# Performance work log

Measured on AMD Instinct MI355X. Metric: run time of the kernel, lower is better.

The kernel has to match this reference:

```python
import jax, jax.numpy as jnp
import numpy as np
from jax import lax

DIM = 192
HEADS = 4
EPS = 1e-12  # torch F.normalize eps


def setup_inputs() -> dict:
    key = jax.random.key(0)
    k1, k2, k3, k4 = jax.random.split(key, 4)
    b, c, h, w = 8, DIM, 128, 128
    x = jax.random.normal(k1, (b, c, h, w), dtype=jnp.float32)
    w_qkv = jax.random.normal(k2, (3 * c, c), dtype=jnp.float32) * (1.0 / np.sqrt(c))
    w_dw = jax.random.normal(k3, (3 * c, 1, 3, 3), dtype=jnp.float32) * (1.0 / 3.0)
    temperature = jnp.ones((HEADS, 1, 1), dtype=jnp.float32)
    w_proj = jax.random.normal(k4, (c, c), dtype=jnp.float32) * (1.0 / np.sqrt(c))
    return {"x": x, "w_qkv": w_qkv, "w_dw": w_dw, "temperature": temperature, "w_proj": w_proj}


def _l2norm(t):
    # torch F.normalize(dim=-1): t / max(||t||_2, eps)
    n = jnp.sqrt(jnp.sum(t * t, axis=-1, keepdims=True))
    return t / jnp.maximum(n, EPS)


def reference(x, w_qkv, w_dw, temperature, w_proj):
    b, c, h, w = x.shape
    heads = HEADS
    hc = c // heads  # channels per head
    # 1x1 conv: dim -> 3*dim
    qkv = jnp.einsum('bchw,oc->bohw', x, w_qkv)
    # depthwise 3x3 conv, padding=1, no relu/norm
    qkv = lax.conv_general_dilated(
        qkv, w_dw, window_strides=(1, 1), padding='SAME',
        feature_group_count=3 * c,
        dimension_numbers=('NCHW', 'OIHW', 'NCHW'))
    q, k, v = jnp.split(qkv, 3, axis=1)
    # b (head c) h w -> b head c (h w)
    n = h * w
    q = q.reshape(b, heads, hc, n)
    k = k.reshape(b, heads, hc, n)
    v = v.reshape(b, heads, hc, n)
    q = _l2norm(q)
    k = _l2norm(k)
    # channel attention: [b, head, hc, hc]
    attn = jnp.einsum('bhcn,bhdn->bhcd', q, k) * temperature[None]
    attn = jax.nn.softmax(attn, axis=-1)
    out = jnp.einsum('bhcd,bhdn->bhcn', attn, v)
    out = out.reshape(b, c, h, w)
    out = jnp.einsum('bchw,oc->bohw', out, w_proj)
    return out
```

## Files before the change

kernel.cpp:

```cpp
#include <hip/hip_runtime.h>
#include <stdint.h>


typedef __attribute__((ext_vector_type(8))) short bf16x8;
typedef __attribute__((ext_vector_type(4))) float f32x4;
typedef __attribute__((ext_vector_type(2))) float f32x2;
typedef __attribute__((ext_vector_type(4))) unsigned int u32x4;
typedef __attribute__((ext_vector_type(2))) unsigned int u32x2;
typedef unsigned short u16;

#define HW 16384
#define CD 192
#define O3 576
#define KD 192

__device__ __forceinline__ float b2f(u16 u) {
    union { unsigned int i; float f; } v; v.i = ((unsigned int)u) << 16; return v.f;
}
__device__ __forceinline__ u16 f2b(float f) {
    union { float f; unsigned int i; } v; v.f = f;
    return (u16)((v.i + 0x7fffu + ((v.i >> 16) & 1u)) >> 16);
}

__global__ __launch_bounds__(256) void fill_f32(float* p, long long n, float val) {
    long long stride = (long long)gridDim.x * 256;
    for (long long i = blockIdx.x * 256LL + threadIdx.x; i < n; i += stride) p[i] = val;
}

__global__ __launch_bounds__(256) void zerof(float* p, int n) {
    int i = blockIdx.x * 256 + threadIdx.x;
    if (i < n) p[i] = 0.f;
}

__global__ __launch_bounds__(256) void afrag_prep(
    const float* __restrict__ W, u16* __restrict__ Af, int M, int NF)
{
    int t = blockIdx.x * 256 + threadIdx.x;
    if (t >= NF * 64) return;
    int F = t >> 6, lane = t & 63;
    int ks = F % 6, mt = (F / 6) & 3, rwmb = F / 24;
    int row = rwmb * 64 + mt * 16 + (lane & 15);
    int k0 = ks * 32 + (lane >> 4) * 8;
    u16 v[8] __attribute__((aligned(16)));
    if (row < M) {
        const float* src = W + (long long)row * KD + k0;
#pragma unroll
        for (int j = 0; j < 8; j++) v[j] = f2b(src[j]);
    } else {
#pragma unroll
        for (int j = 0; j < 8; j++) v[j] = 0;
    }
    *(bf16x8*)&Af[(long long)F * 512 + lane * 8] = *(const bf16x8*)v;
}

template <bool SRC_F32, bool OUT_F32, int NMS>
__global__ __launch_bounds__(256, 2) void gemm_tn(
    const u16* __restrict__ Afrag, const void* __restrict__ Bsrc, void* __restrict__ Cv,
    long long af_bs, long long b_bs, long long c_bs)
{
    __shared__ u16 lsB[128 * 192];
    const int tid = threadIdx.x, lane = tid & 63, wid = tid >> 6;
    const int n0 = blockIdx.x * 128;
    const long long bz = blockIdx.z;
    const int lr = lane & 15, quad = lane >> 4;
    const int wn = wid & 1, wm = wid >> 1;

#define LADDR(n_, ks_) ((n_) * 192 + (((ks_) ^ (((n_) >> 2) & 7)) * 8))

    if (SRC_F32) {
        const int c32 = lane & 31, rs = lane >> 5;
        const float* gp = (const float*)Bsrc + bz * b_bs + n0 + 4 * c32;
        f32x4 bufA[8], bufB[8];
#define LOADC_F(buf, c) do { \
    const float* p_ = gp + (long long)((c) * 64 + wid * 16 + rs * 8) * HW; \
    _Pragma("unroll") for (int i_ = 0; i_ < 8; i_++) \
        buf[i_] = *(const f32x4*)(p_ + (long long)i_ * HW); \
} while (0)
#define PROC_F(buf, c) do { \
    const int kslot_ = (c) * 8 + wid * 2 + rs; \
    _Pragma("unroll") for (int j_ = 0; j_ < 4; j_++) { \
        const int n_ = 4 * c32 + j_; \
        unsigned int p0_, p1_, p2_, p3_; \
        asm("v_cvt_pk_bf16_f32 %0, %1, %2" : "=v"(p0_) : "v"(buf[0][j_]), "v"(buf[1][j_])); \
        asm("v_cvt_pk_bf16_f32 %0, %1, %2" : "=v"(p1_) : "v"(buf[2][j_]), "v"(buf[3][j_])); \
        asm("v_cvt_pk_bf16_f32 %0, %1, %2" : "=v"(p2_) : "v"(buf[4][j_]), "v"(buf[5][j_])); \
        asm("v_cvt_pk_bf16_f32 %0, %1, %2" : "=v"(p3_) : "v"(buf[6][j_]), "v"(buf[7][j_])); \
        *(u32x4*)&lsB[LADDR(n_, kslot_)] = (u32x4){p0_, p1_, p2_, p3_}; \
    } \
} while (0)
        LOADC_F(bufA, 0);
        LOADC_F(bufB, 1);
        __builtin_amdgcn_sched_barrier(0);
        PROC_F(bufA, 0);
        LOADC_F(bufA, 2);
        __builtin_amdgcn_sched_barrier(0);
        PROC_F(bufB, 1);
        PROC_F(bufA, 2);
#undef LOADC_F
#undef PROC_F
    } else {
        const int c16 = lane & 15, rs4 = lane >> 4;
        const u16* gp = (const u16*)Bsrc + bz * b_bs + n0 + 8 * c16;
        u32x4 bufA[4], bufB[4];
#define LOADC_B(buf, c) do { \
    const u16* p_ = gp + (long long)((c) * 64 + wid * 16 + rs4 * 4) * HW; \
    _Pragma("unroll") for (int i_ = 0; i_ < 4; i_++) \
        buf[i_] = *(const u32x4*)(p_ + (long long)i_ * HW); \
} while (0)
#define PROC_B(buf, c) do { \
    const int kslot_ = (c) * 8 + wid * 2 + (rs4 >> 1); \
    const int kh_ = (rs4 & 1) * 4; \
    _Pragma("unroll") for (int j_ = 0; j_ < 4; j_++) { \
        unsigned int l0_ = __builtin_amdgcn_perm(buf[0][j_], buf[1][j_], 0x01000504u); \
        unsigned int l1_ = __builtin_amdgcn_perm(buf[2][j_], buf[3][j_], 0x01000504u); \
        unsigned int h0_ = __builtin_amdgcn_perm(buf[0][j_], buf[1][j_], 0x03020706u); \
        unsigned int h1_ = __builtin_amdgcn_perm(buf[2][j_], buf[3][j_], 0x03020706u); \
        *(u32x2*)&lsB[LADDR(8 * c16 + 2 * j_, kslot_) + kh_] = (u32x2){l0_, l1_}; \
        *(u32x2*)&lsB[LADDR(8 * c16 + 2 * j_ + 1, kslot_) + kh_] = (u32x2){h0_, h1_}; \
    } \
} while (0)
        LOADC_B(bufA, 0);
        LOADC_B(bufB, 1);
        __builtin_amdgcn_sched_barrier(0);
        PROC_B(bufA, 0);
        LOADC_B(bufA, 2);
        __builtin_amdgcn_sched_barrier(0);
        PROC_B(bufB, 1);
        PROC_B(bufA, 2);
#undef LOADC_B
#undef PROC_B
    }
    __syncthreads();

    bf16x8 bfv[6][4];
#pragma unroll
    for (int ks = 0; ks < 6; ks++)
#pragma unroll
        for (int nt = 0; nt < 4; nt++) {
            const int n_ = wn * 64 + nt * 16 + lr;
            bfv[ks][nt] = *(const bf16x8*)&lsB[LADDR(n_, ks * 4 + quad)];
        }
#undef LADDR
    __syncthreads();

    const u16* ApBase = Afrag + bz * af_bs + lane * 8;
    const long long cB = bz * c_bs + n0 + wn * 64;
    constexpr int NT = NMS / 2;

#define LOAD_AF(dst, sv) do { \
    _Pragma("unroll") for (int mtl_ = 0; mtl_ < 2; mtl_++) \
    _Pragma("unroll") for (int ks_ = 0; ks_ < 6; ks_++) \
        dst[mtl_][ks_] = *(const bf16x8*)(ApBase + \
            (long long)(((sv) >> 1) * 24 + (((sv) & 1) * 2 + mtl_) * 6 + ks_) * 512); \
} while (0)
#define COMPUTE_MB(afb, sv) do { \
    f32x4 acc_[2][4]; \
    _Pragma("unroll") for (int i_ = 0; i_ < 2; i_++) \
    _Pragma("unroll") for (int j_ = 0; j_ < 4; j_++) \
        acc_[i_][j_] = (f32x4){0.f, 0.f, 0.f, 0.f}; \
    _Pragma("unroll") for (int ks_ = 0; ks_ < 6; ks_++) \
    _Pragma("unroll") for (int mtl_ = 0; mtl_ < 2; mtl_++) \
    _Pragma("unroll") for (int nt_ = 0; nt_ < 4; nt_++) \
        acc_[mtl_][nt_] = __builtin_amdgcn_mfma_f32_16x16x32_bf16( \
            afb[mtl_][ks_], bfv[ks_][nt_], acc_[mtl_][nt_], 0, 0, 0); \
     \
    if (OUT_F32) { \
        float* sl_ = (float*)lsB + wid * 2304;   \
        _Pragma("unroll") for (int mtl_ = 0; mtl_ < 2; mtl_++) \
        _Pragma("unroll") for (int r_ = 0; r_ < 4; r_++) { \
            const int row_ = mtl_ * 16 + quad * 4 + r_; \
            const int qx_ = (row_ >> 2) & 3; \
            _Pragma("unroll") for (int nt_ = 0; nt_ < 4; nt_++) \
                sl_[row_ * 72 + ((nt_ ^ qx_) * 16 + lr)] = acc_[mtl_][nt_][r_]; \
        } \
        asm volatile("s_waitcnt lgkmcnt(0)" ::: "memory"); \
        __builtin_amdgcn_sched_barrier(0); \
        _Pragma("unroll") for (int p_ = 0; p_ < 8; p_++) { \
            const int rr_ = (lane >> 4) + 4 * p_; \
            const int c4_ = (lane & 15) * 4; \
            const int pc_ = (((c4_ >> 4) ^ ((rr_ >> 2) & 3)) * 16) + (c4_ & 15); \
            f32x4 v_ = *(const f32x4*)&sl_[rr_ * 72 + pc_]; \
            *(f32x4*)&((float*)Cv)[cB + (long long)(32 * (sv) + rr_) * HW + c4_] = v_; \
        } \
    } else { \
        u16* sl_ = lsB + wid * 2304;   \
        _Pragma("unroll") for (int mtl_ = 0; mtl_ < 2; mtl_++) \
        _Pragma("unroll") for (int r_ = 0; r_ < 4; r_++) { \
            const int row_ = mtl_ * 16 + quad * 4 + r_; \
            const int qx_ = (row_ >> 2) & 3; \
            _Pragma("unroll") for (int nt_ = 0; nt_ < 4; nt_++) \
                sl_[row_ * 72 + ((nt_ ^ qx_) * 16 + lr)] = f2b(acc_[mtl_][nt_][r_]); \
        } \
        asm volatile("s_waitcnt lgkmcnt(0)" ::: "memory"); \
        __builtin_amdgcn_sched_barrier(0); \
        _Pragma("unroll") for (int p_ = 0; p_ < 4; p_++) { \
            const int rr_ = (lane >> 3) + 8 * p_; \
            const int c8_ = (lane & 7) * 8; \
            const int pc_ = (((c8_ >> 4) ^ ((rr_ >> 2) & 3)) * 16) + (c8_ & 15); \
            bf16x8 v_ = *(const bf16x8*)&sl_[rr_ * 72 + pc_]; \
            *(bf16x8*)&((u16*)Cv)[cB + (long long)(32 * (sv) + rr_) * HW + c8_] = v_; \
        } \
    } \
} while (0)

    bf16x8 afA[2][6], afB[2][6];
    const int s0 = wm * NT;
    LOAD_AF(afA, s0);
#pragma unroll
    for (int t = 0; t < NT; ++t) {
        if (t + 1 < NT) {
            if (t & 1) LOAD_AF(afA, s0 + t + 1);
            else       LOAD_AF(afB, s0 + t + 1);
            __builtin_amdgcn_sched_barrier(0);
        }
        if (t & 1) COMPUTE_MB(afB, s0 + t);
        else       COMPUTE_MB(afA, s0 + t);
    }
#undef LOAD_AF
#undef COMPUTE_MB
}

__global__ __launch_bounds__(256) void dwconv2(
    const u16* __restrict__ in, const float* __restrict__ wdw, u16* __restrict__ outp,
    long long in_bs, long long out_bs, int wch0)
{
    const int rt = blockIdx.x, ch = blockIdx.y, tid = threadIdx.x;
    const long long bz = blockIdx.z;
    const u16* ip = in + bz * in_bs + (long long)ch * HW;
    u16* op = outp + bz * out_bs + (long long)ch * HW;
    __shared__ float t[18 * 132];
    const int r0 = rt * 16;
    if (tid < 18) {
        t[tid * 132 + 0] = 0.f;   t[tid * 132 + 129] = 0.f;
        t[tid * 132 + 130] = 0.f; t[tid * 132 + 131] = 0.f;
    }
    for (int i = tid; i < 288; i += 256) {
        int rr = i >> 4, cc = (i & 15) * 8;
        int gr = r0 + rr - 1;
        float f[8];
        if (gr >= 0 && gr < 128) {
            bf16x8 v = *(const bf16x8*)(ip + gr * 128 + cc);
#pragma unroll
            for (int j = 0; j < 8; j++) f[j] = b2f((u16)v[j]);
        } else {
#pragma unroll
            for (int j = 0; j < 8; j++) f[j] = 0.f;
        }
#pragma unroll
        for (int j = 0; j < 8; j++) t[rr * 132 + 1 + cc + j] = f[j];
    }
    float w[9];
#pragma unroll
    for (int j = 0; j < 9; j++) w[j] = wdw[(wch0 + ch) * 9 + j];
    __syncthreads();
    const int rr = tid >> 4, c8 = (tid & 15) * 8;
    float o[8] = {0.f, 0.f, 0.f, 0.f, 0.f, 0.f, 0.f, 0.f};
#pragma unroll
    for (int dy = 0; dy < 3; dy++) {
        const float* row = &t[(rr + dy) * 132 + c8];
        float r[12] __attribute__((aligned(16)));
        *(f32x4*)&r[0] = *(const f32x4*)row;
        *(f32x4*)&r[4] = *(const f32x4*)(row + 4);
        *(f32x4*)&r[8] = *(const f32x4*)(row + 8);
        const float w0 = w[dy * 3], w1 = w[dy * 3 + 1], w2 = w[dy * 3 + 2];
#pragma unroll
        for (int j = 0; j < 8; j++) o[j] += w0 * r[j] + w1 * r[j + 1] + w2 * r[j + 2];
    }
    u16 ob[8] __attribute__((aligned(16)));
#pragma unroll
    for (int j = 0; j < 8; j++) ob[j] = f2b(o[j]);
    *(bf16x8*)&op[(long long)(r0 + rr) * 128 + c8] = *(const bf16x8*)ob;
}

__global__ __launch_bounds__(256) void attn_scores(
    const u16* __restrict__ qk, float* __restrict__ S, float* __restrict__ norms,
    int bh0)
{
    const int tid = threadIdx.x, lane = tid & 63, wid = tid >> 6;
    const int kc = blockIdx.x, head = blockIdx.y;
    const long long bz = blockIdx.z;
    const u16* q = qk + bz * (2LL * CD * HW) + (long long)head * 48 * HW;
    const u16* k = q + (long long)CD * HW;
    const int lr = lane & 15, quad = lane >> 4;

    f32x4 sc[3][3], sq[3], sk[3];
#pragma unroll
    for (int i = 0; i < 3; i++) {
#pragma unroll
        for (int j = 0; j < 3; j++) sc[i][j] = (f32x4){0.f, 0.f, 0.f, 0.f};
        sq[i] = (f32x4){0.f, 0.f, 0.f, 0.f};
        sk[i] = (f32x4){0.f, 0.f, 0.f, 0.f};
    }
    const int n0 = kc * 1024 + wid * 256;
#pragma unroll 2
    for (int s = 0; s < 8; s++) {
        const int n = n0 + s * 32 + quad * 8;
        bf16x8 aq[3], ak[3];
#pragma unroll
        for (int t3 = 0; t3 < 3; t3++) {
            aq[t3] = *(const bf16x8*)(q + (long long)(t3 * 16 + lr) * HW + n);
            ak[t3] = *(const bf16x8*)(k + (long long)(t3 * 16 + lr) * HW + n);
        }
#pragma unroll
        for (int mt = 0; mt < 3; mt++)
#pragma unroll
            for (int nt = 0; nt < 3; nt++)
                sc[mt][nt] = __builtin_amdgcn_mfma_f32_16x16x32_bf16(aq[mt], ak[nt], sc[mt][nt], 0, 0, 0);
#pragma unroll
        for (int t3 = 0; t3 < 3; t3++) {
            sq[t3] = __builtin_amdgcn_mfma_f32_16x16x32_bf16(aq[t3], aq[t3], sq[t3], 0, 0, 0);
            sk[t3] = __builtin_amdgcn_mfma_f32_16x16x32_bf16(ak[t3], ak[t3], sk[t3], 0, 0, 0);
        }
    }
    __shared__ float sS[2304];
    __shared__ float snq[48], snk[48];
    for (int i = tid; i < 2304; i += 256) sS[i] = 0.f;
    if (tid < 48) { snq[tid] = 0.f; snk[tid] = 0.f; }
    __syncthreads();
#pragma unroll
    for (int mt = 0; mt < 3; mt++)
#pragma unroll
        for (int nt = 0; nt < 3; nt++)
#pragma unroll
            for (int r = 0; r < 4; r++)
                atomicAdd(&sS[(mt * 16 + quad * 4 + r) * 48 + nt * 16 + lr], sc[mt][nt][r]);
#pragma unroll
    for (int t3 = 0; t3 < 3; t3++)
#pragma unroll
        for (int r = 0; r < 4; r++) {
            int rw = quad * 4 + r;
            if (rw == lr) {
                atomicAdd(&snq[t3 * 16 + rw], sq[t3][r]);
                atomicAdd(&snk[t3 * 16 + rw], sk[t3][r]);
            }
        }
    __syncthreads();
    const int bh = bh0 + (int)bz * 4 + head;
    float* Sg = S + (long long)bh * 2304;
    for (int i = tid; i < 2304; i += 256) atomicAdd(&Sg[i], sS[i]);
    float* ng = norms + bh * 96;
    if (tid < 48) atomicAdd(&ng[tid], snq[tid]);
    else if (tid < 96) atomicAdd(&ng[tid], snk[tid - 48]);
}

__global__ __launch_bounds__(64) void softmax_k(
    const float* __restrict__ S, const float* __restrict__ norms,
    const float* __restrict__ temp, float* __restrict__ attn, int bh0)
{
    const int bh = bh0 + blockIdx.x, head = bh & 3, r = threadIdx.x;
    if (r >= 48) return;
    const float tv = temp[head];
    const float* Sg = S + (long long)bh * 2304;
    const float* ng = norms + bh * 96;
    const float nq = fmaxf(sqrtf(ng[r]), 1e-12f);
    float lg[48];
    float mx = -1e30f;
#pragma unroll
    for (int d = 0; d < 48; d++) {
        float nk = fmaxf(sqrtf(ng[48 + d]), 1e-12f);
        float v = Sg[r * 48 + d] * tv / (nq * nk);
        lg[d] = v; mx = fmaxf(mx, v);
    }
    float sum = 0.f;
#pragma unroll
    for (int d = 0; d < 48; d++) { float e = __expf(lg[d] - mx); lg[d] = e; sum += e; }
    const float inv = 1.f / sum;
    float* Ag = attn + (long long)bh * 2304 + r * 48;
#pragma unroll
    for (int d = 0; d < 48; d++) Ag[d] = lg[d] * inv;
}

__global__ __launch_bounds__(256) void mproj(
    const float* __restrict__ wproj, const float* __restrict__ attn, u16* __restrict__ Mm,
    int b0)
{
    const int ob = blockIdx.x, b = b0 + blockIdx.y, tid = threadIdx.x;
    __shared__ float sA[9216];
    const float* Ab = attn + (long long)b * 9216;
    for (int i = tid; i < 9216; i += 256) sA[i] = Ab[i];
    __syncthreads();
    for (int i = tid; i < 48 * 192; i += 256) {
        int o = ob * 48 + i / 192;
        int cc = i % 192;
        int h = cc / 48, d = cc - h * 48;
        const float* wr = wproj + o * 192 + h * 48;
        const float* ar = &sA[h * 2304 + d];
        float acc = 0.f;
        for (int c = 0; c < 48; c++) acc += wr[c] * ar[c * 48];
        int fi = (o >> 6) * 24 + ((o >> 4) & 3) * 6 + (cc >> 5);
        int lanei = ((cc >> 3) & 3) * 16 + (o & 15);
        Mm[(long long)b * 49152 + (long long)fi * 512 + lanei * 8 + (cc & 7)] = f2b(acc);
    }
}

extern "C" void kernel_launch(void* const* d_in, const int* in_sizes, int n_in,
                              void* d_out, int out_size, void* d_ws, size_t ws_size,
                              hipStream_t stream)
{
    const float* x     = (const float*)d_in[0];
    const float* wqkv  = (const float*)d_in[1];
    const float* wdw   = (const float*)d_in[2];
    const float* temp  = (const float*)d_in[3];
    const float* wproj = (const float*)d_in[4];
    float* out = (float*)d_out;
    char* ws = (char*)d_ws;
    const long long CHW = (long long)CD * HW;

    if (ws_size < 2097152ULL + 31457280ULL) {
        fill_f32<<<2048, 256, 0, stream>>>(out, out_size, 100.0f);
        return;
    }
    int G = 8;
    while (G > 1 && (unsigned long long)(2097152ULL + (unsigned long long)G * 31457280ULL) > (unsigned long long)ws_size)
        G >>= 1;

    float* S      = (float*)ws;
    float* norms  = (float*)(ws + 294912);
    float* attn   = (float*)(ws + 307200);
    u16*   MmF    = (u16*)(ws + 602112);
    u16*   wqkvF  = (u16*)(ws + 1388544);
    u16* region1  = (u16*)(ws + 2097152);
    u16* qkv_pre  = region1 + (long long)G * 2 * CHW;

    zerof<<<300, 256, 0, stream>>>(S, 76800);
    afrag_prep<<<60, 256, 0, stream>>>(wqkv, wqkvF, O3, 240);

    for (int g0 = 0; g0 < 8; g0 += G) {
        gemm_tn<true, false, 18><<<dim3(128, 1, G), 256, 0, stream>>>(
            wqkvF, x + (long long)g0 * CHW, qkv_pre, 0LL, CHW, 3LL * CHW);
        dwconv2<<<dim3(8, 384, G), 256, 0, stream>>>(
            qkv_pre, wdw, region1, 3LL * CHW, 2LL * CHW, 0);
        dwconv2<<<dim3(8, 192, G), 256, 0, stream>>>(
            qkv_pre + 2LL * CHW, wdw, qkv_pre, 3LL * CHW, 3LL * CHW, 384);
        attn_scores<<<dim3(16, 4, G), 256, 0, stream>>>(region1, S, norms, g0 * 4);
        softmax_k<<<4 * G, 64, 0, stream>>>(S, norms, temp, attn, g0 * 4);
        mproj<<<dim3(4, G), 256, 0, stream>>>(wproj, attn, MmF, g0);
        gemm_tn<false, true, 6><<<dim3(128, 1, G), 256, 0, stream>>>(
            MmF + (long long)g0 * 49152, qkv_pre, out + (long long)g0 * CHW,
            49152LL, 3LL * CHW, CHW);
    }
}
```

Baseline: 392.4 us.

## Enlarge dwconv row tiles and replace global atomic score accumulation with partials

The depthwise conv now processes 64-row tiles per block instead of 16, so the halo rows are reloaded less often and fewer blocks are launched. This costs more LDS per block, which may lower occupancy. The attention-score kernel now writes per-chunk partial score and norm buffers into the unused pre-conv k region of the workspace instead of doing global atomicAdds. The softmax kernel sums the 16 partials itself, which also removes the zeroing kernel.

```diff
diff --git a/kernel.cpp b/kernel.cpp
--- a/kernel.cpp
+++ b/kernel.cpp
@@ -13,6 +13,7 @@
 #define CD 192
 #define O3 576
 #define KD 192
+#define CHWE (192LL * 16384LL)
 
 __device__ __forceinline__ float b2f(u16 u) {
     union { unsigned int i; float f; } v; v.i = ((unsigned int)u) << 16; return v.f;
@@ -25,11 +26,6 @@
 __global__ __launch_bounds__(256) void fill_f32(float* p, long long n, float val) {
     long long stride = (long long)gridDim.x * 256;
     for (long long i = blockIdx.x * 256LL + threadIdx.x; i < n; i += stride) p[i] = val;
-}
-
-__global__ __launch_bounds__(256) void zerof(float* p, int n) {
-    int i = blockIdx.x * 256 + threadIdx.x;
-    if (i < n) p[i] = 0.f;
 }
 
 __global__ __launch_bounds__(256) void afrag_prep(
@@ -228,13 +224,13 @@
     const long long bz = blockIdx.z;
     const u16* ip = in + bz * in_bs + (long long)ch * HW;
     u16* op = outp + bz * out_bs + (long long)ch * HW;
-    __shared__ float t[18 * 132];
-    const int r0 = rt * 16;
-    if (tid < 18) {
+    __shared__ float t[66 * 132];
+    const int r0 = rt * 64;
+    if (tid < 66) {
         t[tid * 132 + 0] = 0.f;   t[tid * 132 + 129] = 0.f;
         t[tid * 132 + 130] = 0.f; t[tid * 132 + 131] = 0.f;
     }
-    for (int i = tid; i < 288; i += 256) {
+    for (int i = tid; i < 1056; i += 256) {
         int rr = i >> 4, cc = (i & 15) * 8;
         int gr = r0 + rr - 1;
         float f[8];
@@ -253,28 +249,31 @@
 #pragma unroll
     for (int j = 0; j < 9; j++) w[j] = wdw[(wch0 + ch) * 9 + j];
     __syncthreads();
-    const int rr = tid >> 4, c8 = (tid & 15) * 8;
-    float o[8] = {0.f, 0.f, 0.f, 0.f, 0.f, 0.f, 0.f, 0.f};
-#pragma unroll
-    for (int dy = 0; dy < 3; dy++) {
-        const float* row = &t[(rr + dy) * 132 + c8];
-        float r[12] __attribute__((aligned(16)));
-        *(f32x4*)&r[0] = *(const f32x4*)row;
-        *(f32x4*)&r[4] = *(const f32x4*)(row + 4);
-        *(f32x4*)&r[8] = *(const f32x4*)(row + 8);
-        const float w0 = w[dy * 3], w1 = w[dy * 3 + 1], w2 = w[dy * 3 + 2];
-#pragma unroll
-        for (int j = 0; j < 8; j++) o[j] += w0 * r[j] + w1 * r[j + 1] + w2 * r[j + 2];
-    }
-    u16 ob[8] __attribute__((aligned(16)));
-#pragma unroll
-    for (int j = 0; j < 8; j++) ob[j] = f2b(o[j]);
-    *(bf16x8*)&op[(long long)(r0 + rr) * 128 + c8] = *(const bf16x8*)ob;
+    const int rr0 = tid >> 4, c8 = (tid & 15) * 8;
+#pragma unroll
+    for (int j4 = 0; j4 < 4; j4++) {
+        const int row = rr0 + j4 * 16;
+        float o[8] = {0.f, 0.f, 0.f, 0.f, 0.f, 0.f, 0.f, 0.f};
+#pragma unroll
+        for (int dy = 0; dy < 3; dy++) {
+            const float* rowp = &t[(row + dy) * 132 + c8];
+            float r[12] __attribute__((aligned(16)));
+            *(f32x4*)&r[0] = *(const f32x4*)rowp;
+            *(f32x4*)&r[4] = *(const f32x4*)(rowp + 4);
+            *(f32x4*)&r[8] = *(const f32x4*)(rowp + 8);
+            const float w0 = w[dy * 3], w1 = w[dy * 3 + 1], w2 = w[dy * 3 + 2];
+#pragma unroll
+            for (int j = 0; j < 8; j++) o[j] += w0 * r[j] + w1 * r[j + 1] + w2 * r[j + 2];
+        }
+        u16 ob[8] __attribute__((aligned(16)));
+#pragma unroll
+        for (int j = 0; j < 8; j++) ob[j] = f2b(o[j]);
+        *(bf16x8*)&op[(long long)(r0 + row) * 128 + c8] = *(const bf16x8*)ob;
+    }
 }
 
 __global__ __launch_bounds__(256) void attn_scores(
-    const u16* __restrict__ qk, float* __restrict__ S, float* __restrict__ norms,
-    int bh0)
+    const u16* __restrict__ qk, u16* __restrict__ qkvb)
 {
     const int tid = threadIdx.x, lane = tid & 63, wid = tid >> 6;
     const int kc = blockIdx.x, head = blockIdx.y;
@@ -335,39 +334,59 @@
             }
         }
     __syncthreads();
-    const int bh = bh0 + (int)bz * 4 + head;
-    float* Sg = S + (long long)bh * 2304;
-    for (int i = tid; i < 2304; i += 256) atomicAdd(&Sg[i], sS[i]);
-    float* ng = norms + bh * 96;
-    if (tid < 48) atomicAdd(&ng[tid], snq[tid]);
-    else if (tid < 96) atomicAdd(&ng[tid], snk[tid - 48]);
-}
-
-__global__ __launch_bounds__(64) void softmax_k(
-    const float* __restrict__ S, const float* __restrict__ norms,
-    const float* __restrict__ temp, float* __restrict__ attn, int bh0)
-{
-    const int bh = bh0 + blockIdx.x, head = bh & 3, r = threadIdx.x;
-    if (r >= 48) return;
-    const float tv = temp[head];
-    const float* Sg = S + (long long)bh * 2304;
-    const float* ng = norms + bh * 96;
-    const float nq = fmaxf(sqrtf(ng[r]), 1e-12f);
-    float lg[48];
-    float mx = -1e30f;
-#pragma unroll
-    for (int d = 0; d < 48; d++) {
-        float nk = fmaxf(sqrtf(ng[48 + d]), 1e-12f);
-        float v = Sg[r * 48 + d] * tv / (nq * nk);
-        lg[d] = v; mx = fmaxf(mx, v);
-    }
-    float sum = 0.f;
-#pragma unroll
-    for (int d = 0; d < 48; d++) { float e = __expf(lg[d] - mx); lg[d] = e; sum += e; }
-    const float inv = 1.f / sum;
-    float* Ag = attn + (long long)bh * 2304 + r * 48;
-#pragma unroll
-    for (int d = 0; d < 48; d++) Ag[d] = lg[d] * inv;
+    float* Pb = (float*)(qkvb + bz * 3 * CHWE + CHWE);
+    float* Sp = Pb + head * 36864 + kc * 2304;
+    float* Np = Pb + 147456 + head * 1536 + kc * 96;
+    for (int i = tid; i < 2304; i += 256) Sp[i] = sS[i];
+    if (tid < 48) Np[tid] = snq[tid];
+    else if (tid < 96) Np[tid] = snk[tid - 48];
+}
+
+__global__ __launch_bounds__(256) void softmax_k(
+    const u16* __restrict__ qkvb, const float* __restrict__ temp,
+    float* __restrict__ attn, int bh0)
+{
+    const int tid = threadIdx.x, bx = blockIdx.x;
+    const int head = bx & 3, bloc = bx >> 2;
+    const int bh = bh0 + bx;
+    const float* Pb = (const float*)(qkvb + (long long)bloc * 3 * CHWE + CHWE);
+    const float* Sp = Pb + head * 36864;
+    const float* Np = Pb + 147456 + head * 1536;
+    __shared__ float Ssum[2304];
+    __shared__ float Nsum[96];
+    for (int i = tid; i < 2304; i += 256) {
+        float s = 0.f;
+#pragma unroll
+        for (int kc = 0; kc < 16; kc++) s += Sp[kc * 2304 + i];
+        Ssum[i] = s;
+    }
+    if (tid < 96) {
+        float s = 0.f;
+#pragma unroll
+        for (int kc = 0; kc < 16; kc++) s += Np[kc * 96 + tid];
+        Nsum[tid] = s;
+    }
+    __syncthreads();
+    if (tid < 48) {
+        const int r = tid;
+        const float tv = temp[head];
+        const float nq = fmaxf(sqrtf(Nsum[r]), 1e-12f);
+        float lg[48];
+        float mx = -1e30f;
+#pragma unroll
+        for (int d = 0; d < 48; d++) {
+            float nk = fmaxf(sqrtf(Nsum[48 + d]), 1e-12f);
+            float v = Ssum[r * 48 + d] * tv / (nq * nk);
+            lg[d] = v; mx = fmaxf(mx, v);
+        }
+        float sum = 0.f;
+#pragma unroll
+        for (int d = 0; d < 48; d++) { float e = __expf(lg[d] - mx); lg[d] = e; sum += e; }
+        const float inv = 1.f / sum;
+        float* Ag = attn + (long long)bh * 2304 + r * 48;
+#pragma unroll
+        for (int d = 0; d < 48; d++) Ag[d] = lg[d] * inv;
+    }
 }
 
 __global__ __launch_bounds__(256) void mproj(
@@ -404,7 +423,7 @@
     const float* wproj = (const float*)d_in[4];
     float* out = (float*)d_out;
     char* ws = (char*)d_ws;
-    const long long CHW = (long long)CD * HW;
+    const long long CHW = CHWE;
 
     if (ws_size < 2097152ULL + 31457280ULL) {
         fill_f32<<<2048, 256, 0, stream>>>(out, out_size, 100.0f);
@@ -414,26 +433,23 @@
     while (G > 1 && (unsigned long long)(2097152ULL + (unsigned long long)G * 31457280ULL) > (unsigned long long)ws_size)
         G >>= 1;
 
-    float* S      = (float*)ws;
-    float* norms  = (float*)(ws + 294912);
     float* attn   = (float*)(ws + 307200);
     u16*   MmF    = (u16*)(ws + 602112);
     u16*   wqkvF  = (u16*)(ws + 1388544);
     u16* region1  = (u16*)(ws + 2097152);
     u16* qkv_pre  = region1 + (long long)G * 2 * CHW;
 
-    zerof<<<300, 256, 0, stream>>>(S, 76800);
     afrag_prep<<<60, 256, 0, stream>>>(wqkv, wqkvF, O3, 240);
 
     for (int g0 = 0; g0 < 8; g0 += G) {
         gemm_tn<true, false, 18><<<dim3(128, 1, G), 256, 0, stream>>>(
             wqkvF, x + (long long)g0 * CHW, qkv_pre, 0LL, CHW, 3LL * CHW);
-        dwconv2<<<dim3(8, 384, G), 256, 0, stream>>>(
+        dwconv2<<<dim3(2, 384, G), 256, 0, stream>>>(
             qkv_pre, wdw, region1, 3LL * CHW, 2LL * CHW, 0);
-        dwconv2<<<dim3(8, 192, G), 256, 0, stream>>>(
+        dwconv2<<<dim3(2, 192, G), 256, 0, stream>>>(
             qkv_pre + 2LL * CHW, wdw, qkv_pre, 3LL * CHW, 3LL * CHW, 384);
-        attn_scores<<<dim3(16, 4, G), 256, 0, stream>>>(region1, S, norms, g0 * 4);
-        softmax_k<<<4 * G, 64, 0, stream>>>(S, norms, temp, attn, g0 * 4);
+        attn_scores<<<dim3(16, 4, G), 256, 0, stream>>>(region1, qkv_pre);
+        softmax_k<<<4 * G, 256, 0, stream>>>(qkv_pre, temp, attn, g0 * 4);
         mproj<<<dim3(4, G), 256, 0, stream>>>(wproj, attn, MmF, g0);
         gemm_tn<false, true, 6><<<dim3(128, 1, G), 256, 0, stream>>>(
             MmF + (long long)g0 * 49152, qkv_pre, out + (long long)g0 * CHW,
```

New measurement: 398.2 us. No clear change (+1.5%).
